# Kernel optimization log

Hardware: AMD Instinct MI355X
Metric: run time of the kernel (lower is better)

Reference implementation:

```python
import jax, jax.numpy as jnp
jax.config.update("jax_enable_x64", True)  # original computes in float64
import numpy as np

ALPHA = 0.01  # init kwarg


def setup_inputs() -> dict:
    key = jax.random.key(0)
    x = jax.random.normal(key, (8, 8192, 512), dtype=jnp.float32)
    return {"x": x}


def reference(x):
    # x: [B, T, C]
    _, t, _ = x.shape
    # powers = flip(arange(t)) = [t-1, t-2, ..., 0]
    powers = jnp.arange(t - 1, -1, -1, dtype=jnp.float64)
    base = jnp.power(1.0 - ALPHA, powers)          # (1-alpha)^(t-1-i), [T]
    divisor = base.reshape(1, t, 1)                # [1, T, 1]
    weights = base.at[1:].multiply(ALPHA).reshape(1, t, 1)
    out = jnp.cumsum(x.astype(jnp.float64) * weights, axis=1) / divisor
    return out.astype(x.dtype)
```

## Files before the change

kernel.cpp:

```cpp
#include <hip/hip_runtime.h>
#include <math.h>


namespace {
constexpr int B = 8;
constexpr int T = 8192;
constexpr int C = 512;
constexpr float ALPHA = 0.01f;
constexpr float DECAY = 1.0f - ALPHA;
constexpr int CHUNK = 128;
constexpr int K = T / CHUNK;
constexpr int STRIDE4 = C / 4;
constexpr int TPB = C / 4;
}

__global__ __launch_bounds__(TPB) void ema_ends_kernel(const float* __restrict__ x,
                                                       float* __restrict__ ends) {
    const int k = blockIdx.x;
    const int b = blockIdx.y;
    const int tid = threadIdx.x;
    const float4* xp = reinterpret_cast<const float4*>(x) +
                       (size_t)(b * T + k * CHUNK) * STRIDE4 + tid;
    float4 y;
    if (k == 0) {
        y = xp[0];
    } else {
        y = make_float4(0.f, 0.f, 0.f, 0.f);
    }
#pragma unroll 8
    for (int t = 0; t < CHUNK; ++t) {
        float4 v = xp[(size_t)t * STRIDE4];
        y.x = DECAY * y.x + ALPHA * v.x;
        y.y = DECAY * y.y + ALPHA * v.y;
        y.z = DECAY * y.z + ALPHA * v.z;
        y.w = DECAY * y.w + ALPHA * v.w;
    }
    reinterpret_cast<float4*>(ends)[(size_t)(b * K + k) * STRIDE4 + tid] = y;
}

__global__ __launch_bounds__(TPB) void ema_scan_kernel(const float* __restrict__ x,
                                                       const float* __restrict__ ends,
                                                       float* __restrict__ out,
                                                       float decay_chunk) {
    const int k = blockIdx.x;
    const int b = blockIdx.y;
    const int tid = threadIdx.x;
    const size_t base4 = (size_t)(b * T + k * CHUNK) * STRIDE4 + tid;
    const float4* xp = reinterpret_cast<const float4*>(x) + base4;
    float4* op = reinterpret_cast<float4*>(out) + base4;

    float4 y;
    if (k == 0) {
        y = xp[0];
    } else {
        y = make_float4(0.f, 0.f, 0.f, 0.f);
        const float4* ep = reinterpret_cast<const float4*>(ends) +
                           (size_t)b * K * STRIDE4 + tid;
        for (int m = 0; m < k; ++m) {
            float4 e = ep[(size_t)m * STRIDE4];
            y.x = decay_chunk * y.x + e.x;
            y.y = decay_chunk * y.y + e.y;
            y.z = decay_chunk * y.z + e.z;
            y.w = decay_chunk * y.w + e.w;
        }
    }
#pragma unroll 4
    for (int t = 0; t < CHUNK; ++t) {
        float4 v = xp[(size_t)t * STRIDE4];
        y.x = DECAY * y.x + ALPHA * v.x;
        y.y = DECAY * y.y + ALPHA * v.y;
        y.z = DECAY * y.z + ALPHA * v.z;
        y.w = DECAY * y.w + ALPHA * v.w;
        op[(size_t)t * STRIDE4] = y;
    }
}

__global__ __launch_bounds__(TPB) void ema_seq_kernel(const float* __restrict__ x,
                                                      float* __restrict__ out) {
    const int b = blockIdx.x;
    const int tid = threadIdx.x;
    const float4* xp = reinterpret_cast<const float4*>(x) + (size_t)b * T * STRIDE4 + tid;
    float4* op = reinterpret_cast<float4*>(out) + (size_t)b * T * STRIDE4 + tid;
    float4 y = xp[0];
    for (int t = 0; t < T; ++t) {
        float4 v = xp[(size_t)t * STRIDE4];
        y.x = DECAY * y.x + ALPHA * v.x;
        y.y = DECAY * y.y + ALPHA * v.y;
        y.z = DECAY * y.z + ALPHA * v.z;
        y.w = DECAY * y.w + ALPHA * v.w;
        op[(size_t)t * STRIDE4] = y;
    }
}

extern "C" void kernel_launch(void* const* d_in, const int* in_sizes, int n_in,
                              void* d_out, int out_size, void* d_ws, size_t ws_size,
                              hipStream_t stream) {
    (void)in_sizes; (void)n_in; (void)out_size;
    const float* x = reinterpret_cast<const float*>(d_in[0]);
    float* out = reinterpret_cast<float*>(d_out);

    const size_t ws_need = (size_t)B * K * C * sizeof(float);
    const float decay_chunk = (float)pow((double)DECAY, (double)CHUNK);

    if (ws_size >= ws_need) {
        float* ends = reinterpret_cast<float*>(d_ws);
        ema_ends_kernel<<<dim3(K, B), dim3(TPB), 0, stream>>>(x, ends);
        ema_scan_kernel<<<dim3(K, B), dim3(TPB), 0, stream>>>(x, ends, out, decay_chunk);
    } else {
        ema_seq_kernel<<<dim3(B), dim3(TPB), 0, stream>>>(x, out);
    }
}
```

Baseline: 261.8 us.

## Split EMA into chunk-ends, serial carry scan, and apply passes with smaller chunks

Replaces the per-block quadratic re-scan of preceding chunk ends with a separate carry kernel. One block per batch scans the chunk ends sequentially and writes each chunk's incoming state in place. Chunk size drops from 128 to 32, giving more blocks for parallelism, and the output stores become nontemporal. This adds a third launch and a serial carry pass over 256 chunks per batch that runs on only 8 blocks.

Result: slower. 272.4 us (+4.1%).

```diff
diff --git a/kernel.cpp b/kernel.cpp
--- a/kernel.cpp
+++ b/kernel.cpp
@@ -8,19 +8,28 @@
 constexpr int C = 512;
 constexpr float ALPHA = 0.01f;
 constexpr float DECAY = 1.0f - ALPHA;
-constexpr int CHUNK = 128;
-constexpr int K = T / CHUNK;
-constexpr int STRIDE4 = C / 4;
-constexpr int TPB = C / 4;
+constexpr int S4 = C / 4;
+constexpr int TPB = S4;
+
+typedef float f32x4 __attribute__((ext_vector_type(4)));
+
+__device__ __forceinline__ void ema_step(float4& y, const float4 v) {
+    y.x = DECAY * y.x + ALPHA * v.x;
+    y.y = DECAY * y.y + ALPHA * v.y;
+    y.z = DECAY * y.z + ALPHA * v.z;
+    y.w = DECAY * y.w + ALPHA * v.w;
+}
 }
 
-__global__ __launch_bounds__(TPB) void ema_ends_kernel(const float* __restrict__ x,
-                                                       float* __restrict__ ends) {
+template <int CHUNK>
+__global__ __launch_bounds__(TPB) void ema_ends(const float* __restrict__ x,
+                                                float* __restrict__ ends) {
+    constexpr int K = T / CHUNK;
     const int k = blockIdx.x;
     const int b = blockIdx.y;
     const int tid = threadIdx.x;
     const float4* xp = reinterpret_cast<const float4*>(x) +
-                       (size_t)(b * T + k * CHUNK) * STRIDE4 + tid;
+                       (size_t)(b * T + k * CHUNK) * S4 + tid;
     float4 y;
     if (k == 0) {
         y = xp[0];
@@ -29,23 +38,39 @@
     }
 #pragma unroll 8
     for (int t = 0; t < CHUNK; ++t) {
-        float4 v = xp[(size_t)t * STRIDE4];
-        y.x = DECAY * y.x + ALPHA * v.x;
-        y.y = DECAY * y.y + ALPHA * v.y;
-        y.z = DECAY * y.z + ALPHA * v.z;
-        y.w = DECAY * y.w + ALPHA * v.w;
+        float4 v = xp[(size_t)t * S4];
+        ema_step(y, v);
     }
-    reinterpret_cast<float4*>(ends)[(size_t)(b * K + k) * STRIDE4 + tid] = y;
+    reinterpret_cast<float4*>(ends)[(size_t)(b * K + k) * S4 + tid] = y;
 }
 
-__global__ __launch_bounds__(TPB) void ema_scan_kernel(const float* __restrict__ x,
-                                                       const float* __restrict__ ends,
-                                                       float* __restrict__ out,
-                                                       float decay_chunk) {
+template <int CHUNK>
+__global__ __launch_bounds__(TPB) void ema_carry(float* ends, float dC) {
+    constexpr int K = T / CHUNK;
+    const int b = blockIdx.x;
+    const int tid = threadIdx.x;
+    float4* ep = reinterpret_cast<float4*>(ends) + (size_t)b * K * S4 + tid;
+    float4 y = ep[0];
+#pragma unroll 8
+    for (int m = 1; m < K; ++m) {
+        float4 e = ep[(size_t)m * S4];
+        ep[(size_t)m * S4] = y;
+        y.x = dC * y.x + e.x;
+        y.y = dC * y.y + e.y;
+        y.z = dC * y.z + e.z;
+        y.w = dC * y.w + e.w;
+    }
+}
+
+template <int CHUNK>
+__global__ __launch_bounds__(TPB) void ema_apply(const float* __restrict__ x,
+                                                 const float* __restrict__ carry,
+                                                 float* __restrict__ out) {
+    constexpr int K = T / CHUNK;
     const int k = blockIdx.x;
     const int b = blockIdx.y;
     const int tid = threadIdx.x;
-    const size_t base4 = (size_t)(b * T + k * CHUNK) * STRIDE4 + tid;
+    const size_t base4 = (size_t)(b * T + k * CHUNK) * S4 + tid;
     const float4* xp = reinterpret_cast<const float4*>(x) + base4;
     float4* op = reinterpret_cast<float4*>(out) + base4;
 
@@ -53,25 +78,14 @@
     if (k == 0) {
         y = xp[0];
     } else {
-        y = make_float4(0.f, 0.f, 0.f, 0.f);
-        const float4* ep = reinterpret_cast<const float4*>(ends) +
-                           (size_t)b * K * STRIDE4 + tid;
-        for (int m = 0; m < k; ++m) {
-            float4 e = ep[(size_t)m * STRIDE4];
-            y.x = decay_chunk * y.x + e.x;
-            y.y = decay_chunk * y.y + e.y;
-            y.z = decay_chunk * y.z + e.z;
-            y.w = decay_chunk * y.w + e.w;
-        }
+        y = reinterpret_cast<const float4*>(carry)[(size_t)(b * K + k) * S4 + tid];
     }
-#pragma unroll 4
+#pragma unroll 8
     for (int t = 0; t < CHUNK; ++t) {
-        float4 v = xp[(size_t)t * STRIDE4];
-        y.x = DECAY * y.x + ALPHA * v.x;
-        y.y = DECAY * y.y + ALPHA * v.y;
-        y.z = DECAY * y.z + ALPHA * v.z;
-        y.w = DECAY * y.w + ALPHA * v.w;
-        op[(size_t)t * STRIDE4] = y;
+        float4 v = xp[(size_t)t * S4];
+        ema_step(y, v);
+        __builtin_nontemporal_store(*reinterpret_cast<const f32x4*>(&y),
+                                    reinterpret_cast<f32x4*>(op + (size_t)t * S4));
     }
 }
 
@@ -79,16 +93,13 @@
                                                       float* __restrict__ out) {
     const int b = blockIdx.x;
     const int tid = threadIdx.x;
-    const float4* xp = reinterpret_cast<const float4*>(x) + (size_t)b * T * STRIDE4 + tid;
-    float4* op = reinterpret_cast<float4*>(out) + (size_t)b * T * STRIDE4 + tid;
+    const float4* xp = reinterpret_cast<const float4*>(x) + (size_t)b * T * S4 + tid;
+    float4* op = reinterpret_cast<float4*>(out) + (size_t)b * T * S4 + tid;
     float4 y = xp[0];
     for (int t = 0; t < T; ++t) {
-        float4 v = xp[(size_t)t * STRIDE4];
-        y.x = DECAY * y.x + ALPHA * v.x;
-        y.y = DECAY * y.y + ALPHA * v.y;
-        y.z = DECAY * y.z + ALPHA * v.z;
-        y.w = DECAY * y.w + ALPHA * v.w;
-        op[(size_t)t * STRIDE4] = y;
+        float4 v = xp[(size_t)t * S4];
+        ema_step(y, v);
+        op[(size_t)t * S4] = y;
     }
 }
 
@@ -99,13 +110,26 @@
     const float* x = reinterpret_cast<const float*>(d_in[0]);
     float* out = reinterpret_cast<float*>(d_out);
 
-    const size_t ws_need = (size_t)B * K * C * sizeof(float);
-    const float decay_chunk = (float)pow((double)DECAY, (double)CHUNK);
+    constexpr int CH = 32;
+    constexpr int KCH = T / CH;
+    const size_t need = (size_t)B * KCH * C * sizeof(float);
 
-    if (ws_size >= ws_need) {
+    constexpr int CH2 = 128;
+    constexpr int KCH2 = T / CH2;
+    const size_t need2 = (size_t)B * KCH2 * C * sizeof(float);
+
+    if (ws_size >= need) {
         float* ends = reinterpret_cast<float*>(d_ws);
-        ema_ends_kernel<<<dim3(K, B), dim3(TPB), 0, stream>>>(x, ends);
-        ema_scan_kernel<<<dim3(K, B), dim3(TPB), 0, stream>>>(x, ends, out, decay_chunk);
+        const float dC = (float)pow((double)DECAY, (double)CH);
+        ema_ends<CH><<<dim3(KCH, B), dim3(TPB), 0, stream>>>(x, ends);
+        ema_carry<CH><<<dim3(B), dim3(TPB), 0, stream>>>(ends, dC);
+        ema_apply<CH><<<dim3(KCH, B), dim3(TPB), 0, stream>>>(x, ends, out);
+    } else if (ws_size >= need2) {
+        float* ends = reinterpret_cast<float*>(d_ws);
+        const float dC = (float)pow((double)DECAY, (double)CH2);
+        ema_ends<CH2><<<dim3(KCH2, B), dim3(TPB), 0, stream>>>(x, ends);
+        ema_carry<CH2><<<dim3(B), dim3(TPB), 0, stream>>>(ends, dC);
+        ema_apply<CH2><<<dim3(KCH2, B), dim3(TPB), 0, stream>>>(x, ends, out);
     } else {
         ema_seq_kernel<<<dim3(B), dim3(TPB), 0, stream>>>(x, out);
     }
```
